# Performance work log

Measured on AMD Instinct MI355X. Metric: run time of the kernel, lower is better.

The kernel has to match this reference:

```python
import jax, jax.numpy as jnp
import numpy as np

B, N, D_IN, D_OUT = 2, 4096, 768, 768


def setup_inputs() -> dict:
    key = jax.random.key(0)
    kx, kq, kk, kv = jax.random.split(key, 4)
    x = jax.random.normal(kx, (B, N, D_IN), dtype=jnp.float32)
    # Linear(d_in, d_out, bias=False) weights, stored as [d_in, d_out]
    scale = 1.0 / np.sqrt(D_IN)
    Wq = jax.random.normal(kq, (D_IN, D_OUT), dtype=jnp.float32) * scale
    Wk = jax.random.normal(kk, (D_IN, D_OUT), dtype=jnp.float32) * scale
    Wv = jax.random.normal(kv, (D_IN, D_OUT), dtype=jnp.float32) * scale
    return {"x": x, "Wq": Wq, "Wk": Wk, "Wv": Wv}


def reference(x, Wq, Wk, Wv):
    # q,k,v: [B, N, D_OUT]
    q = jnp.einsum('bnd,de->bne', x, Wq)
    k = jnp.einsum('bnd,de->bne', x, Wk)
    v = jnp.einsum('bnd,de->bne', x, Wv)
    # Full [B, N, N] score matrix (naive attention, as in source).
    # NOTE: source's masked_fill is non-in-place and discarded, so NO causal
    # mask is actually applied -- reproduced faithfully here.
    scores = jnp.einsum('bqe,bke->bqk', q, k) / jnp.sqrt(jnp.float32(k.shape[-1]))
    weights = jax.nn.softmax(scores, axis=-1)
    # dropout rate 0.0 / eval mode -> identity
    out = jnp.einsum('bqk,bke->bqe', weights, v)  # [B, N, D_OUT]
    return out
```

## Files before the change

kernel.cpp:

```cpp
#include <hip/hip_runtime.h>

typedef __bf16 bf16x8 __attribute__((ext_vector_type(8)));
typedef float f32x4 __attribute__((ext_vector_type(4)));
typedef unsigned short us8 __attribute__((ext_vector_type(8)));

#define GAS __attribute__((address_space(1)))
#define LAS __attribute__((address_space(3)))

__device__ __forceinline__ unsigned short f32_to_bf16(float f) {
    unsigned int u = __float_as_uint(f);
    u += 0x7FFFu + ((u >> 16) & 1u);
    return (unsigned short)(u >> 16);
}

__device__ __forceinline__ float bf16_to_f32(unsigned short h) {
    return __uint_as_float((unsigned int)h << 16);
}

__device__ __forceinline__ void load16(const unsigned short* g, unsigned short* l) {
    __builtin_amdgcn_global_load_lds((GAS unsigned int*)g, (LAS unsigned int*)l, 16, 0, 0);
}

__global__ __launch_bounds__(1024) void prep(
    const float* __restrict__ x, unsigned short* __restrict__ Xbf,
    const float* __restrict__ W0, const float* __restrict__ W1, const float* __restrict__ W2,
    unsigned short* __restrict__ T0, unsigned short* __restrict__ T1, unsigned short* __restrict__ T2,
    float* __restrict__ lsum)
{
    __shared__ float tile[32][33];
    const int id = blockIdx.x;
    const int t = threadIdx.x;
    if (id < 1536) {
        int i = id * 1024 + t;
        float4 v = ((const float4*)x)[i];
        ushort4 o;
        o.x = f32_to_bf16(v.x); o.y = f32_to_bf16(v.y);
        o.z = f32_to_bf16(v.z); o.w = f32_to_bf16(v.w);
        ((ushort4*)Xbf)[i] = o;
    } else if (id < 3264) {
        const int tid = id - 1536;
        const int z = tid / 576, rem = tid % 576;
        const int by = rem / 24, bx = rem % 24;
        const float* W = (z == 0) ? W0 : (z == 1) ? W1 : W2;
        unsigned short* T = (z == 0) ? T0 : (z == 1) ? T1 : T2;
        const int r0 = by * 32, c0 = bx * 32;
        const int tx = t & 31, ty = t >> 5;
        tile[ty][tx] = W[(size_t)(r0 + ty) * 768 + c0 + tx];
        __syncthreads();
        T[(size_t)(c0 + ty) * 768 + r0 + tx] = f32_to_bf16(tile[tx][ty]);
    } else {
        float4 z4 = {0.f, 0.f, 0.f, 0.f};
        ((float4*)lsum)[t] = z4;
        ((float4*)lsum)[t + 1024] = z4;
    }
}

__global__ __launch_bounds__(256) void qkv_proj(
    const unsigned short* __restrict__ Xbf,
    const unsigned short* __restrict__ Wt,
    unsigned short* __restrict__ QK,
    unsigned short* __restrict__ Vt)
{
    const int id = blockIdx.x;
    const unsigned short* A; const unsigned short* B;
    unsigned short* C; int ldc, m0, n0;
    if (id < 768) {
        const int z = id / 384, r = id % 384;
        A = Xbf; B = Wt + (size_t)z * 589824; C = QK + (size_t)z * 6291456;
        ldc = 768;
        m0 = (r / 6) * 128; n0 = (r % 6) * 128;
    } else {
        const int j = id - 768;
        A = Wt + 1179648ull;
        B = Xbf; C = Vt;
        ldc = 8192;
        m0 = (j >> 6) * 128; n0 = (j & 63) * 128;
    }
    const int lda = 768, ldb = 768;
    const int t = threadIdx.x;
    const int lane = t & 63;
    const int w = t >> 6;
    const int wm = (w >> 1) * 64;
    const int wn = (w & 1) * 64;

    __shared__ unsigned short At[128 * 64];
    __shared__ unsigned short Bt[128 * 64];

    f32x4 acc[4][4];
#pragma unroll
    for (int i = 0; i < 4; ++i)
#pragma unroll
        for (int j2 = 0; j2 < 4; ++j2) acc[i][j2] = (f32x4){0.f, 0.f, 0.f, 0.f};

    const int r15 = lane & 15;
    const int qa = lane >> 4;

    for (int k0 = 0; k0 < 768; k0 += 64) {
#pragma unroll
        for (int i = 0; i < 4; ++i) {
            const int c = i * 256 + t;
            const int row = c >> 3;
            const int cc = (c & 7) ^ (row & 7);
            load16(A + (size_t)(m0 + row) * lda + k0 + cc * 8, &At[c * 8]);
            load16(B + (size_t)(n0 + row) * ldb + k0 + cc * 8, &Bt[c * 8]);
        }
        __syncthreads();

#pragma unroll
        for (int ks = 0; ks < 2; ++ks) {
            bf16x8 af[4], bf[4];
#pragma unroll
            for (int mi = 0; mi < 4; ++mi) {
                const int row = wm + mi * 16 + r15;
                af[mi] = *(const bf16x8*)&At[row * 64 + (((ks << 2) + qa) ^ (row & 7)) * 8];
            }
#pragma unroll
            for (int ni = 0; ni < 4; ++ni) {
                const int row = wn + ni * 16 + r15;
                bf[ni] = *(const bf16x8*)&Bt[row * 64 + (((ks << 2) + qa) ^ (row & 7)) * 8];
            }
#pragma unroll
            for (int mi = 0; mi < 4; ++mi)
#pragma unroll
                for (int ni = 0; ni < 4; ++ni)
                    acc[mi][ni] = __builtin_amdgcn_mfma_f32_16x16x32_bf16(
                        af[mi], bf[ni], acc[mi][ni], 0, 0, 0);
        }
        __syncthreads();
    }

    const int cr = (lane >> 4) * 4;
#pragma unroll
    for (int mi = 0; mi < 4; ++mi)
#pragma unroll
        for (int ni = 0; ni < 4; ++ni) {
            const int gm = m0 + wm + mi * 16 + cr;
            const int gn = n0 + wn + ni * 16 + r15;
#pragma unroll
            for (int r = 0; r < 4; ++r)
                C[(size_t)(gm + r) * ldc + gn] = f32_to_bf16(acc[mi][ni][r]);
        }
}

__global__ __launch_bounds__(512, 2) void gemm_s_exp2(
    const unsigned short* __restrict__ Q, const unsigned short* __restrict__ Kb,
    unsigned short* __restrict__ Sexp, float* __restrict__ lsum, float alpha)
{
    const int f = blockIdx.x;
    const int xcd = f & 7;
    const int local = f >> 3;
    const int x = (xcd & 1) * 8 + (local & 7);
    const int y = ((xcd >> 1) & 1) * 8 + (local >> 3);
    const int bb = xcd >> 2;
    const unsigned short* A = Q + (size_t)bb * 3145728;
    const unsigned short* B = Kb + (size_t)bb * 3145728;
    unsigned short* C = Sexp + (size_t)bb * 16777216;
    float* ls = lsum + bb * 4096;
    const int m0 = y * 256, n0 = x * 256;
    const int lda = 768, ldb = 768, ldc = 4096;
    constexpr int NT = 12;

    __shared__ unsigned short As[2][256 * 64];
    __shared__ unsigned short Bs[2][256 * 64];

    const int t = threadIdx.x;
    const int lane = t & 63;
    const int w = t >> 6;
    const int wm = (w >> 2) * 128;
    const int wn = (w & 3) * 64;
    const int r15 = lane & 15;
    const int qa = lane >> 4;

    const unsigned short* srcA[4];
    const unsigned short* srcB[4];
    int dst[4];
#pragma unroll
    for (int i = 0; i < 4; ++i) {
        const int c = i * 512 + t;
        const int row = c >> 3;
        const int cc = (c & 7) ^ (row & 7);
        srcA[i] = A + (size_t)(m0 + row) * lda + cc * 8;
        srcB[i] = B + (size_t)(n0 + row) * ldb + cc * 8;
        dst[i] = c * 8;
    }

    auto stage = [&](int buf, int kbase) {
#pragma unroll
        for (int i = 0; i < 4; ++i)
            load16(srcA[i] + kbase, &As[buf][dst[i]]);
#pragma unroll
        for (int i = 0; i < 4; ++i)
            load16(srcB[i] + kbase, &Bs[buf][dst[i]]);
    };

    int offA[8][2], offB[4][2];
#pragma unroll
    for (int mi = 0; mi < 8; ++mi) {
        const int row = wm + mi * 16 + r15;
#pragma unroll
        for (int ks = 0; ks < 2; ++ks)
            offA[mi][ks] = row * 64 + (((ks << 2) + qa) ^ (row & 7)) * 8;
    }
#pragma unroll
    for (int ni = 0; ni < 4; ++ni) {
        const int row = wn + ni * 16 + r15;
#pragma unroll
        for (int ks = 0; ks < 2; ++ks)
            offB[ni][ks] = row * 64 + (((ks << 2) + qa) ^ (row & 7)) * 8;
    }

    f32x4 acc[8][4];
#pragma unroll
    for (int i = 0; i < 8; ++i)
#pragma unroll
        for (int j = 0; j < 4; ++j) acc[i][j] = (f32x4){0.f, 0.f, 0.f, 0.f};

    stage(0, 0);
    stage(1, 64);

    for (int tt = 0; tt < NT; ++tt) {
        const int b = tt & 1;
        if (tt == NT - 1) {
            asm volatile("s_waitcnt vmcnt(0)" ::: "memory");
        } else {
            asm volatile("s_waitcnt vmcnt(8)" ::: "memory");
        }
        __builtin_amdgcn_s_barrier();

#pragma unroll
        for (int ks = 0; ks < 2; ++ks) {
            bf16x8 aA[8], bB[4];
#pragma unroll
            for (int i = 0; i < 8; ++i)
                aA[i] = *(const bf16x8*)&As[b][offA[i][ks]];
#pragma unroll
            for (int ni = 0; ni < 4; ++ni)
                bB[ni] = *(const bf16x8*)&Bs[b][offB[ni][ks]];
#pragma unroll
            for (int i = 0; i < 8; ++i)
#pragma unroll
                for (int ni = 0; ni < 4; ++ni)
                    acc[i][ni] = __builtin_amdgcn_mfma_f32_16x16x32_bf16(
                        aA[i], bB[ni], acc[i][ni], 0, 0, 0);
        }

        asm volatile("" ::: "memory");
        __builtin_amdgcn_s_barrier();

        if (tt + 2 < NT) stage(b, (tt + 2) << 6);
    }

    const int cr = (lane >> 4) * 4;
#pragma unroll
    for (int mi = 0; mi < 8; ++mi)
#pragma unroll
        for (int ni = 0; ni < 4; ++ni) {
            const int gm = m0 + wm + mi * 16 + cr;
            const int gn = n0 + wn + ni * 16 + r15;
#pragma unroll
            for (int r = 0; r < 4; ++r)
                C[(size_t)(gm + r) * ldc + gn] =
                    f32_to_bf16(__expf(alpha * acc[mi][ni][r]));
        }

    asm volatile("s_waitcnt vmcnt(0)" ::: "memory");
    __builtin_amdgcn_s_barrier();

    {
        const int row = t >> 1;
        const unsigned short* rp =
            C + (size_t)(m0 + row) * ldc + n0 + (t & 1) * 128;
        float s = 0.f;
#pragma unroll
        for (int i = 0; i < 16; ++i) {
            us8 v = ((const us8*)rp)[i];
#pragma unroll
            for (int j = 0; j < 8; ++j) s += bf16_to_f32(v[j]);
        }
        s += __shfl_xor(s, 1, 64);
        if ((t & 1) == 0) atomicAdd(&ls[m0 + row], s);
    }
}

__global__ __launch_bounds__(512, 2) void gemm_out(
    const unsigned short* __restrict__ P, const unsigned short* __restrict__ Vt,
    const float* __restrict__ lsum, float* __restrict__ out)
{
    const int f = blockIdx.x;
    const int xcd = f & 7;
    const int batch = xcd >> 2;
    const int nb = xcd & 3;
    const int mb = f >> 3;
    const unsigned short* A = P + (size_t)batch * 16777216;
    const unsigned short* B = Vt + (size_t)batch * 4096;
    const float* ls = lsum + batch * 4096;
    float* C = out + (size_t)batch * 3145728;
    const int m0 = mb * 128, n0 = nb * 192;
    const int lda = 4096, ldb = 8192;
    constexpr int NT = 64;

    __shared__ unsigned short As[3][128 * 64];
    __shared__ unsigned short Bs[3][192 * 64];

    const int t = threadIdx.x;
    const int lane = t & 63;
    const int w = t >> 6;
    const int wm = (w >> 2) * 64;
    const int wn = (w & 3) * 48;
    const int r15 = lane & 15;
    const int qa = lane >> 4;

    const unsigned short* srcA[2];
    int dstA[2];
#pragma unroll
    for (int i = 0; i < 2; ++i) {
        const int c = i * 512 + t;
        const int row = c >> 3;
        const int cc = (c & 7) ^ (row & 7);
        srcA[i] = A + (size_t)(m0 + row) * lda + cc * 8;
        dstA[i] = c * 8;
    }
    const unsigned short* srcB[3];
    int dstB[3];
#pragma unroll
    for (int i = 0; i < 3; ++i) {
        const int c = i * 512 + t;
        const int row = c >> 3;
        const int cc = (c & 7) ^ (row & 7);
        srcB[i] = B + (size_t)(n0 + row) * ldb + cc * 8;
        dstB[i] = c * 8;
    }

    auto stage = [&](int buf, int kbase) {
#pragma unroll
        for (int i = 0; i < 2; ++i)
            load16(srcA[i] + kbase, &As[buf][dstA[i]]);
#pragma unroll
        for (int i = 0; i < 3; ++i)
            load16(srcB[i] + kbase, &Bs[buf][dstB[i]]);
    };

    int offA[4][2], offB[3][2];
#pragma unroll
    for (int mi = 0; mi < 4; ++mi) {
        const int row = wm + mi * 16 + r15;
#pragma unroll
        for (int ks = 0; ks < 2; ++ks)
            offA[mi][ks] = row * 64 + (((ks << 2) + qa) ^ (row & 7)) * 8;
    }
#pragma unroll
    for (int ni = 0; ni < 3; ++ni) {
        const int row = wn + ni * 16 + r15;
#pragma unroll
        for (int ks = 0; ks < 2; ++ks)
            offB[ni][ks] = row * 64 + (((ks << 2) + qa) ^ (row & 7)) * 8;
    }

    f32x4 acc[4][3];
#pragma unroll
    for (int i = 0; i < 4; ++i)
#pragma unroll
        for (int j = 0; j < 3; ++j) acc[i][j] = (f32x4){0.f, 0.f, 0.f, 0.f};

    stage(0, 0);
    stage(1, 64);
    stage(2, 128);

    int b = 0;
    for (int tt = 0; tt < NT; ++tt) {
        if (tt < NT - 2) {
            asm volatile("s_waitcnt vmcnt(10)" ::: "memory");
        } else if (tt == NT - 2) {
            asm volatile("s_waitcnt vmcnt(5)" ::: "memory");
        } else {
            asm volatile("s_waitcnt vmcnt(0)" ::: "memory");
        }
        __builtin_amdgcn_s_barrier();

#pragma unroll
        for (int ks = 0; ks < 2; ++ks) {
            bf16x8 aA[4], bB[3];
#pragma unroll
            for (int i = 0; i < 4; ++i)
                aA[i] = *(const bf16x8*)&As[b][offA[i][ks]];
#pragma unroll
            for (int ni = 0; ni < 3; ++ni)
                bB[ni] = *(const bf16x8*)&Bs[b][offB[ni][ks]];
#pragma unroll
            for (int i = 0; i < 4; ++i)
#pragma unroll
                for (int ni = 0; ni < 3; ++ni)
                    acc[i][ni] = __builtin_amdgcn_mfma_f32_16x16x32_bf16(
                        aA[i], bB[ni], acc[i][ni], 0, 0, 0);
        }

        asm volatile("" ::: "memory");
        __builtin_amdgcn_s_barrier();

        if (tt + 3 < NT) stage(b, (tt + 3) << 6);
        b = (b == 2) ? 0 : b + 1;
    }

    const int cr = (lane >> 4) * 4;
#pragma unroll
    for (int mi = 0; mi < 4; ++mi) {
        const int gm = m0 + wm + mi * 16 + cr;
        const float i0 = 1.f / ls[gm + 0];
        const float i1 = 1.f / ls[gm + 1];
        const float i2 = 1.f / ls[gm + 2];
        const float i3 = 1.f / ls[gm + 3];
#pragma unroll
        for (int ni = 0; ni < 3; ++ni) {
            const int gn = n0 + wn + ni * 16 + r15;
            C[(size_t)(gm + 0) * 768 + gn] = acc[mi][ni][0] * i0;
            C[(size_t)(gm + 1) * 768 + gn] = acc[mi][ni][1] * i1;
            C[(size_t)(gm + 2) * 768 + gn] = acc[mi][ni][2] * i2;
            C[(size_t)(gm + 3) * 768 + gn] = acc[mi][ni][3] * i3;
        }
    }
}

extern "C" void kernel_launch(void* const* d_in, const int* in_sizes, int n_in,
                              void* d_out, int out_size, void* d_ws, size_t ws_size,
                              hipStream_t stream) {
    const float* x  = (const float*)d_in[0];
    const float* Wq = (const float*)d_in[1];
    const float* Wk = (const float*)d_in[2];
    const float* Wv = (const float*)d_in[3];
    float* out = (float*)d_out;

    char* base = (char*)d_ws;
    size_t off = 0;
    auto alloc = [&](size_t b) { char* p = base + off; off += (b + 255) & ~(size_t)255; return p; };

    unsigned short* Xbf = (unsigned short*)alloc(8192ull * 768 * 2);
    unsigned short* WqT = (unsigned short*)alloc(768ull * 768 * 2);
    unsigned short* WkT = (unsigned short*)alloc(768ull * 768 * 2);
    unsigned short* WvT = (unsigned short*)alloc(768ull * 768 * 2);
    unsigned short* Qb  = (unsigned short*)alloc(8192ull * 768 * 2);
    unsigned short* Kb  = (unsigned short*)alloc(8192ull * 768 * 2);
    unsigned short* Vt  = (unsigned short*)alloc(768ull * 8192 * 2);
    unsigned short* Sexp = (unsigned short*)alloc(2ull * 4096 * 4096 * 2);
    float* lsum = (float*)alloc(2ull * 4096 * 4);
    (void)ws_size; (void)in_sizes; (void)n_in; (void)out_size; (void)WkT; (void)WvT;

    prep<<<dim3(3265), dim3(1024), 0, stream>>>(x, Xbf, Wq, Wk, Wv, WqT, WkT, WvT, lsum);
    qkv_proj<<<dim3(1152), dim3(256), 0, stream>>>(Xbf, WqT, Qb, Vt);
    gemm_s_exp2<<<dim3(512), dim3(512), 0, stream>>>(
        Qb, Kb, Sexp, lsum, 0.03608439182435161f);
    gemm_out<<<dim3(256), dim3(512), 0, stream>>>(Sexp, Vt, lsum, out);
}
```

Before: 271.7 us.

## Compute softmax row sums via ones-MFMA in output GEMM, drop separate reduction

Removes the post-store reread and atomic row-sum reduction from the score/exp kernel and the lsum buffer and zeroing. Row sums are instead accumulated in the PV GEMM by an extra MFMA of the P tile against an all-ones vector, reusing data already in LDS. Also remaps gemm_out blocks so the column blocks of a row group share an XCD. This adds extra MFMA work per k-step but avoids a second pass over the large score matrix and the atomics.

```diff
diff --git a/kernel.cpp b/kernel.cpp
--- a/kernel.cpp
+++ b/kernel.cpp
@@ -24,8 +24,7 @@
 __global__ __launch_bounds__(1024) void prep(
     const float* __restrict__ x, unsigned short* __restrict__ Xbf,
     const float* __restrict__ W0, const float* __restrict__ W1, const float* __restrict__ W2,
-    unsigned short* __restrict__ T0, unsigned short* __restrict__ T1, unsigned short* __restrict__ T2,
-    float* __restrict__ lsum)
+    unsigned short* __restrict__ T0, unsigned short* __restrict__ T1, unsigned short* __restrict__ T2)
 {
     __shared__ float tile[32][33];
     const int id = blockIdx.x;
@@ -37,7 +36,7 @@
         o.x = f32_to_bf16(v.x); o.y = f32_to_bf16(v.y);
         o.z = f32_to_bf16(v.z); o.w = f32_to_bf16(v.w);
         ((ushort4*)Xbf)[i] = o;
-    } else if (id < 3264) {
+    } else {
         const int tid = id - 1536;
         const int z = tid / 576, rem = tid % 576;
         const int by = rem / 24, bx = rem % 24;
@@ -48,10 +47,6 @@
         tile[ty][tx] = W[(size_t)(r0 + ty) * 768 + c0 + tx];
         __syncthreads();
         T[(size_t)(c0 + ty) * 768 + r0 + tx] = f32_to_bf16(tile[tx][ty]);
-    } else {
-        float4 z4 = {0.f, 0.f, 0.f, 0.f};
-        ((float4*)lsum)[t] = z4;
-        ((float4*)lsum)[t + 1024] = z4;
     }
 }
 
@@ -144,7 +139,7 @@
 
 __global__ __launch_bounds__(512, 2) void gemm_s_exp2(
     const unsigned short* __restrict__ Q, const unsigned short* __restrict__ Kb,
-    unsigned short* __restrict__ Sexp, float* __restrict__ lsum, float alpha)
+    unsigned short* __restrict__ Sexp, float alpha)
 {
     const int f = blockIdx.x;
     const int xcd = f & 7;
@@ -155,7 +150,6 @@
     const unsigned short* A = Q + (size_t)bb * 3145728;
     const unsigned short* B = Kb + (size_t)bb * 3145728;
     unsigned short* C = Sexp + (size_t)bb * 16777216;
-    float* ls = lsum + bb * 4096;
     const int m0 = y * 256, n0 = x * 256;
     const int lda = 768, ldb = 768, ldc = 4096;
     constexpr int NT = 12;
@@ -262,38 +256,21 @@
                 C[(size_t)(gm + r) * ldc + gn] =
                     f32_to_bf16(__expf(alpha * acc[mi][ni][r]));
         }
-
-    asm volatile("s_waitcnt vmcnt(0)" ::: "memory");
-    __builtin_amdgcn_s_barrier();
-
-    {
-        const int row = t >> 1;
-        const unsigned short* rp =
-            C + (size_t)(m0 + row) * ldc + n0 + (t & 1) * 128;
-        float s = 0.f;
-#pragma unroll
-        for (int i = 0; i < 16; ++i) {
-            us8 v = ((const us8*)rp)[i];
-#pragma unroll
-            for (int j = 0; j < 8; ++j) s += bf16_to_f32(v[j]);
-        }
-        s += __shfl_xor(s, 1, 64);
-        if ((t & 1) == 0) atomicAdd(&ls[m0 + row], s);
-    }
 }
 
 __global__ __launch_bounds__(512, 2) void gemm_out(
     const unsigned short* __restrict__ P, const unsigned short* __restrict__ Vt,
-    const float* __restrict__ lsum, float* __restrict__ out)
+    float* __restrict__ out)
 {
     const int f = blockIdx.x;
     const int xcd = f & 7;
-    const int batch = xcd >> 2;
-    const int nb = xcd & 3;
-    const int mb = f >> 3;
+    const int local = f >> 3;
+    const int nb = local & 3;
+    const int rg = xcd * 8 + (local >> 2);
+    const int batch = rg >> 5;
+    const int mb = rg & 31;
     const unsigned short* A = P + (size_t)batch * 16777216;
     const unsigned short* B = Vt + (size_t)batch * 4096;
-    const float* ls = lsum + batch * 4096;
     float* C = out + (size_t)batch * 3145728;
     const int m0 = mb * 128, n0 = nb * 192;
     const int lda = 4096, ldb = 8192;
@@ -356,11 +333,19 @@
             offB[ni][ks] = row * 64 + (((ks << 2) + qa) ^ (row & 7)) * 8;
     }
 
+    us8 uo;
+#pragma unroll
+    for (int j = 0; j < 8; ++j) uo[j] = 0x3F80;
+    const bf16x8 vones = __builtin_bit_cast(bf16x8, uo);
+
     f32x4 acc[4][3];
-#pragma unroll
-    for (int i = 0; i < 4; ++i)
+    f32x4 acc1[4];
+#pragma unroll
+    for (int i = 0; i < 4; ++i) {
 #pragma unroll
         for (int j = 0; j < 3; ++j) acc[i][j] = (f32x4){0.f, 0.f, 0.f, 0.f};
+        acc1[i] = (f32x4){0.f, 0.f, 0.f, 0.f};
+    }
 
     stage(0, 0);
     stage(1, 64);
@@ -387,11 +372,14 @@
             for (int ni = 0; ni < 3; ++ni)
                 bB[ni] = *(const bf16x8*)&Bs[b][offB[ni][ks]];
 #pragma unroll
-            for (int i = 0; i < 4; ++i)
+            for (int i = 0; i < 4; ++i) {
 #pragma unroll
                 for (int ni = 0; ni < 3; ++ni)
                     acc[i][ni] = __builtin_amdgcn_mfma_f32_16x16x32_bf16(
                         aA[i], bB[ni], acc[i][ni], 0, 0, 0);
+                acc1[i] = __builtin_amdgcn_mfma_f32_16x16x32_bf16(
+                    aA[i], vones, acc1[i], 0, 0, 0);
+            }
         }
 
         asm volatile("" ::: "memory");
@@ -405,10 +393,10 @@
 #pragma unroll
     for (int mi = 0; mi < 4; ++mi) {
         const int gm = m0 + wm + mi * 16 + cr;
-        const float i0 = 1.f / ls[gm + 0];
-        const float i1 = 1.f / ls[gm + 1];
-        const float i2 = 1.f / ls[gm + 2];
-        const float i3 = 1.f / ls[gm + 3];
+        const float i0 = 1.f / acc1[mi][0];
+        const float i1 = 1.f / acc1[mi][1];
+        const float i2 = 1.f / acc1[mi][2];
+        const float i3 = 1.f / acc1[mi][3];
 #pragma unroll
         for (int ni = 0; ni < 3; ++ni) {
             const int gn = n0 + wn + ni * 16 + r15;
@@ -441,12 +429,11 @@
     unsigned short* Kb  = (unsigned short*)alloc(8192ull * 768 * 2);
     unsigned short* Vt  = (unsigned short*)alloc(768ull * 8192 * 2);
     unsigned short* Sexp = (unsigned short*)alloc(2ull * 4096 * 4096 * 2);
-    float* lsum = (float*)alloc(2ull * 4096 * 4);
     (void)ws_size; (void)in_sizes; (void)n_in; (void)out_size; (void)WkT; (void)WvT;
 
-    prep<<<dim3(3265), dim3(1024), 0, stream>>>(x, Xbf, Wq, Wk, Wv, WqT, WkT, WvT, lsum);
+    prep<<<dim3(3264), dim3(1024), 0, stream>>>(x, Xbf, Wq, Wk, Wv, WqT, WkT, WvT);
     qkv_proj<<<dim3(1152), dim3(256), 0, stream>>>(Xbf, WqT, Qb, Vt);
     gemm_s_exp2<<<dim3(512), dim3(512), 0, stream>>>(
-        Qb, Kb, Sexp, lsum, 0.03608439182435161f);
-    gemm_out<<<dim3(256), dim3(512), 0, stream>>>(Sexp, Vt, lsum, out);
-}
+        Qb, Kb, Sexp, 0.03608439182435161f);
+    gemm_out<<<dim3(256), dim3(512), 0, stream>>>(Sexp, Vt, out);
+}
```

Measured after the change: 250.0 us. -8.0%, faster.
